# Optimization experiments

Measured on AMD Instinct MI355X. Metric: run time of the kernel, lower is better.

Reference implementation:

```python
import jax, jax.numpy as jnp
import numpy as np
from jax import lax

N_IN, N_H = 3, 2
N_REC = N_IN + N_H  # 5 qubits in the recurrent cell


def _ry(theta):
    # theta: (B,) -> (B, 2, 2) complex64 RY matrices
    c = jnp.cos(theta * 0.5).astype(jnp.complex64)
    s = jnp.sin(theta * 0.5).astype(jnp.complex64)
    return jnp.stack([jnp.stack([c, -s], -1), jnp.stack([s, c], -1)], -2)


def _rot(phi, theta, omega):
    # PennyLane Rot(phi, theta, omega) = RZ(omega) @ RY(theta) @ RZ(phi)
    c = jnp.cos(theta * 0.5)
    s = jnp.sin(theta * 0.5)
    ep = jnp.exp(-0.5j * (phi + omega))  # e^{-i(phi+omega)/2}
    em = jnp.exp(0.5j * (phi - omega))   # e^{+i(phi-omega)/2}
    m = jnp.stack([jnp.stack([ep * c, -em * s], -1),
                   jnp.stack([jnp.conj(em) * s, jnp.conj(ep) * c], -1)], -2)
    return m.astype(jnp.complex64)


def _apply1q(state, U, wire, n):
    # state: (B, 2**n); wire 0 is most significant (PennyLane convention)
    L, R = 2 ** wire, 2 ** (n - wire - 1)
    st = state.reshape(-1, L, 2, R)
    sub = 'bij,bljr->blir' if U.ndim == 3 else 'ij,bljr->blir'
    return jnp.einsum(sub, U, st).reshape(state.shape)


def _cnot_perm(c, t, n):
    # CNOT is a fixed basis permutation: flip target bit where control bit set
    cbit, tbit = 1 << (n - 1 - c), 1 << (n - 1 - t)
    idx = np.arange(2 ** n)
    return np.where(idx & cbit, idx ^ tbit, idx)


def _entangle(state, weights, n):
    # StronglyEntanglingLayers: per-wire Rot, then CNOT ring with range r
    n_layers = weights.shape[0]
    for l in range(n_layers):
        for w in range(n):
            state = _apply1q(state, _rot(weights[l, w, 0], weights[l, w, 1], weights[l, w, 2]), w, n)
        r = (l % (n - 1)) + 1
        for w in range(n):
            state = state[:, _cnot_perm(w, (w + r) % n, n)]
    return state


def _expz(state, wire, n):
    # <Z_wire> = P(0) - P(1)
    L, R = 2 ** wire, 2 ** (n - wire - 1)
    p = (state.real ** 2 + state.imag ** 2).reshape(-1, L, 2, R).sum((1, 3))
    return p[:, 0] - p[:, 1]


def _init_state(batch, n):
    s = jnp.zeros((batch, 2 ** n), jnp.complex64)
    return s.at[:, 0].set(1.0)


def _cell(x, h, w_rec):
    # batched qrnn_cell: RY-encode x on wires 0..2, h on wires 3..4, entangle, read Z(3),Z(4)
    state = _init_state(x.shape[0], N_REC)
    for i in range(N_IN):
        state = _apply1q(state, _ry(x[:, i]), i, N_REC)
    for j in range(N_H):
        state = _apply1q(state, _ry(h[:, j]), N_IN + j, N_REC)
    state = _entangle(state, w_rec, N_REC)
    return jnp.stack([_expz(state, N_IN + j, N_REC) for j in range(N_H)], -1)


def _readout(h, w_out):
    # batched qnn_readout: 2-qubit circuit, Z(0) expval
    state = _init_state(h.shape[0], N_H)
    for j in range(N_H):
        state = _apply1q(state, _ry(h[:, j]), j, N_H)
    state = _entangle(state, w_out, N_H)
    return _expz(state, 0, N_H)[:, None]


def setup_inputs() -> dict:
    key = jax.random.key(0)
    k1, k2, k3 = jax.random.split(key, 3)
    T, B = 32, 8192
    x_seq = jax.random.normal(k1, (T, B, N_IN), jnp.float32)
    w_rec = jax.random.normal(k2, (2, N_REC, 3), jnp.float32)
    w_out = jax.random.normal(k3, (2, N_H, 3), jnp.float32)
    return {"x_seq": x_seq, "w_rec": w_rec, "w_out": w_out}


def reference(x_seq, w_rec, w_out):
    B = x_seq.shape[1]

    def step(h, xt):
        return _cell(xt, h, w_rec), None

    h, _ = lax.scan(step, jnp.zeros((B, N_H), jnp.float32), x_seq)
    return _readout(h, w_out)  # (B, 1)
```

## Files before the change

### kernel.cpp

```cpp
#include <hip/hip_runtime.h>
#include <math.h>


using f32x2 = __attribute__((ext_vector_type(2))) float;
using f32x4 = __attribute__((ext_vector_type(4))) float;

constexpr int cnot_ct(int idx, int c, int t) {
    return (idx & (1 << (4 - c))) ? (idx ^ (1 << (4 - t))) : idx;
}
constexpr int Pfwd_ct(int x, int r) {
    for (int w = 4; w >= 0; --w) x = cnot_ct(x, w, (w + r) % 5);
    return x;
}
constexpr int Pinv_ct(int x, int r) {
    for (int w = 0; w <= 4; ++w) x = cnot_ct(x, w, (w + r) % 5);
    return x;
}
static_assert(Pinv_ct(Pfwd_ct(13, 1), 1) == 13, "inv1");
static_assert(Pinv_ct(Pfwd_ct(22, 2), 2) == 22, "inv2");

constexpr int GMASK[10] = {16, 8, 4, 2, 1,
                           Pfwd_ct(16,1), Pfwd_ct(8,1), Pfwd_ct(4,1), Pfwd_ct(2,1), Pfwd_ct(1,1)};
constexpr int fmask_l1(int pb) {
    int f = 0;
    for (int b = 0; b < 5; ++b) if ((Pinv_ct(1 << b, 1) >> pb) & 1) f |= 1 << b;
    return f;
}
constexpr int FMASK[10] = {16, 8, 4, 2, 1,
                           fmask_l1(4), fmask_l1(3), fmask_l1(2), fmask_l1(1), fmask_l1(0)};
constexpr int cinv_ct(int x) { return Pinv_ct(Pinv_ct(x, 1), 2); }
constexpr int fmask_fin(int pb) {
    int f = 0;
    for (int b = 0; b < 5; ++b) if ((cinv_ct(1 << b) >> pb) & 1) f |= 1 << b;
    return f;
}
constexpr int SF3 = fmask_fin(1);
constexpr int SF4 = fmask_fin(0);

constexpr bool gates_straddle() {
    for (int g = 0; g < 10; ++g)
        if (!(__builtin_popcount(GMASK[g] & FMASK[g]) & 1)) return false;
    return true;
}
static_assert(gates_straddle(), "GMASK/FMASK straddle");

constexpr unsigned span3_ct(int a, int b, int c) {
    unsigned m = 0;
    for (int i = 0; i < 8; ++i) {
        int v = ((i & 1) ? a : 0) ^ ((i & 2) ? b : 0) ^ ((i & 4) ? c : 0);
        m |= 1u << v;
    }
    return m;
}
static_assert(span3_ct(1, 2, 7) == 0xFFu, "butterfly {1,2,7} spans lanes 0..7");

__device__ __forceinline__ int pinv_rt(int x, int r) {
    #pragma unroll
    for (int w = 0; w < 5; ++w) {
        int cbit = 1 << (4 - w), tbit = 1 << (4 - ((w + r) % 5));
        if (x & cbit) x ^= tbit;
    }
    return x;
}

__device__ __forceinline__ float Wsel(int r, int d) {
    float b, c;
    if (d == 0)      { b =  2.f / 3.f; c = 0.f; }
    else if (d == 1) { b = -1.f / 3.f; c =  0.57735026918962576f; }
    else             { b = -1.f / 3.f; c = -0.57735026918962576f; }
    return (r == 0) ? (1.f / 3.f) : ((r == 1) ? b : c);
}

__device__ __forceinline__ float f4c(const float4& v, int c) {
    return (c == 0) ? v.x : ((c == 1) ? v.y : ((c == 2) ? v.z : v.w));
}

__device__ __forceinline__ f32x2 pkfma(f32x2 a, f32x2 b, f32x2 c) {
    return __builtin_elementwise_fma(a, b, c);
}
__device__ __forceinline__ f32x2 splat2(float v) { return (f32x2){v, v}; }

template<int CTRL> __device__ __forceinline__ float dppf(float x) {
    return __int_as_float(__builtin_amdgcn_mov_dpp(__float_as_int(x), CTRL, 0xF, 0xF, true));
}
template<int PL> __device__ __forceinline__ float mvf(float x) {
    if constexpr (PL == 1)      return dppf<0xB1>(x);
    else if constexpr (PL == 2) return dppf<0x4E>(x);
    else if constexpr (PL == 7) return dppf<0x141>(x);
    else if constexpr (PL == 8) return dppf<0x128>(x);
    else { static_assert(PL == 1 || PL == 2 || PL == 7 || PL == 8, "mask"); return x; }
}

template<int g>
__device__ __forceinline__ void gate_full2(f32x2 (&amp)[32], f32x2 cc, f32x2 ss) {
    constexpr int m = GMASK[g], F = FMASK[g];
    #pragma unroll
    for (int i = 0; i < 32; ++i) {
        if ((__builtin_popcount(i & F) & 1) == 0) {
            const int j = i ^ m;
            const f32x2 v0 = amp[i], v1 = amp[j];
            amp[i] = pkfma(cc, v0, -(ss * v1));
            amp[j] = pkfma(ss, v0,  cc * v1);
        }
    }
}

__global__ __launch_bounds__(512, 2) void qrnn_fused(
    const float* __restrict__ x_seq, const float* __restrict__ w_rec,
    const float* __restrict__ w_out, float* __restrict__ out, int B) {

    __shared__ __align__(16) float4 xs4[32 * 33];
    __shared__ __align__(16) float A2s[18 * 28];
    __shared__ float CgS[10], SgS[10];
    __shared__ float F0c[5], F0s[5];
    __shared__ __align__(8) f32x2 E1cs[32];
    __shared__ float RC[16];
    __shared__ __align__(16) float Cm_pool[32 * 18 * 36];
    float* const Qs  = Cm_pool;
    float* const P1s = Cm_pool + 512;

    const int tloc = threadIdx.x;
    const int grp  = tloc >> 4;
    const int k    = tloc & 15;
    const int b0   = blockIdx.x * 32;
    const int b    = b0 + grp;

    #pragma unroll
    for (int qq = 0; qq < 2; ++qq) {
        const int p = tloc + qq * 512;
        const int ts = p >> 5, lbs = p & 31;
        const int gidx = (ts * B + (b0 + lbs)) * 3;
        float4 v;
        v.x = x_seq[gidx]; v.y = x_seq[gidx + 1]; v.z = x_seq[gidx + 2]; v.w = 0.f;
        xs4[lbs * 33 + ts] = v;
    }

    if (tloc < 10) {
        const float th = w_rec[(tloc / 5) * 15 + (tloc % 5) * 3 + 1];
        CgS[tloc] = cosf(0.5f * th);
        SgS[tloc] = sinf(0.5f * th);
    } else if (tloc >= 16 && tloc < 21) {
        const int w = tloc - 16;
        const float ph = 0.5f * w_rec[w * 3 + 0];
        F0c[w] = cosf(ph); F0s[w] = sinf(ph);
    } else if (tloc >= 64 && tloc < 96) {
        const int i = tloc - 64;
        const int j = pinv_rt(i, 1);
        float ang = 0.f;
        #pragma unroll
        for (int w = 0; w < 5; ++w) {
            ang += (((i >> (4 - w)) & 1) ? 0.5f : -0.5f) * w_rec[w * 3 + 2];
            ang += (((j >> (4 - w)) & 1) ? 0.5f : -0.5f) * w_rec[15 + w * 3 + 0];
        }
        E1cs[i] = (f32x2){cosf(ang), sinf(ang)};
    } else if (tloc >= 96 && tloc < 100) {
        const int g = tloc - 96;
        const int li = g >> 1, w = g & 1;
        const float phi = w_out[li * 6 + w * 3 + 0];
        const float the = w_out[li * 6 + w * 3 + 1];
        const float ome = w_out[li * 6 + w * 3 + 2];
        const float cs = cosf(0.5f * the), ss = sinf(0.5f * the);
        const float cp = cosf(0.5f * (phi + ome)), sp = sinf(0.5f * (phi + ome));
        const float cm = cosf(0.5f * (phi - ome)), sm = sinf(0.5f * (phi - ome));
        RC[g * 4 + 0] = cp * cs;
        RC[g * 4 + 1] = -sp * cs;
        RC[g * 4 + 2] = cm * ss;
        RC[g * 4 + 3] = sm * ss;
    }
    __syncthreads();

    if (tloc < 243) {
        const int dsel[5] = {tloc / 81, (tloc / 27) % 3, (tloc / 9) % 3,
                             (tloc / 3) % 3, tloc % 3};
        constexpr float S3v = 0.86602540378443865f;
        float Arw[5], Aiw[5], Brw[5], Biw[5];
        #pragma unroll
        for (int w = 0; w < 5; ++w) {
            const int d = dsel[w];
            const float fc = (d == 0) ? 1.f : 0.5f;
            const float fs = (d == 0) ? 0.f : ((d == 1) ? S3v : -S3v);
            const float c = CgS[w], s = SgS[w];
            const float t1 = fmaf(c, fc, -s * fs);
            const float t2 = fmaf(c, fc,  s * fs);
            const float t3 = fmaf(s, fc,  c * fs);
            const float t4 = fmaf(c, fs, -s * fc);
            Arw[w] =  F0c[w] * t1;  Aiw[w] = -F0s[w] * t2;
            Brw[w] =  F0c[w] * t3;  Biw[w] =  F0s[w] * t4;
        }
        f32x2 amp[32];
        amp[0] = (f32x2){Arw[0], Aiw[0]};
        amp[1] = (f32x2){Brw[0], Biw[0]};
        #pragma unroll
        for (int w = 1; w < 5; ++w) {
            const int n = 1 << w;
            #pragma unroll
            for (int m = n - 1; m >= 0; --m) {
                const float orr = amp[m].x, oii = amp[m].y;
                amp[2*m]   = (f32x2){fmaf(orr, Arw[w], -oii * Aiw[w]),
                                     fmaf(orr, Aiw[w],  oii * Arw[w])};
                amp[2*m+1] = (f32x2){fmaf(orr, Brw[w], -oii * Biw[w]),
                                     fmaf(orr, Biw[w],  oii * Brw[w])};
            }
        }
        #pragma unroll
        for (int i = 0; i < 32; ++i) {
            const f32x2 e = E1cs[i];
            const f32x2 a = amp[i];
            amp[i] = (f32x2){a.x * e.x - a.y * e.y, a.x * e.y + a.y * e.x};
        }
        {
            const f32x2 c5 = splat2(CgS[5]), s5 = splat2(SgS[5]);
            const f32x2 c6 = splat2(CgS[6]), s6 = splat2(SgS[6]);
            const f32x2 c7 = splat2(CgS[7]), s7 = splat2(SgS[7]);
            const f32x2 c8 = splat2(CgS[8]), s8 = splat2(SgS[8]);
            const f32x2 c9 = splat2(CgS[9]), s9 = splat2(SgS[9]);
            gate_full2<5>(amp, c5, s5);
            gate_full2<6>(amp, c6, s6);
            gate_full2<7>(amp, c7, s7);
            gate_full2<8>(amp, c8, s8);
            gate_full2<9>(amp, c9, s9);
        }
        float q0 = 0.f, q1 = 0.f;
        #pragma unroll
        for (int i = 0; i < 32; ++i) {
            const f32x2 t = amp[i] * amp[i];
            const float p = t.x + t.y;
            q0 += (__builtin_popcount(i & SF3) & 1) ? -p : p;
            q1 += (__builtin_popcount(i & SF4) & 1) ? -p : p;
        }
        *(f32x2*)&Qs[tloc * 2] = (f32x2){q0, q1};
    }
    __syncthreads();

    if (tloc < 243) {
        const int e = tloc;
        const int d012 = e / 9, pq = e % 9, pp = pq / 3, qq2 = pq % 3;
        f32x2 acc = (f32x2){0.f, 0.f};
        #pragma unroll
        for (int d3 = 0; d3 < 3; ++d3) {
            const float wp = Wsel(pp, d3);
            #pragma unroll
            for (int d4 = 0; d4 < 3; ++d4) {
                const float w = wp * Wsel(qq2, d4);
                const f32x2 qp = *(const f32x2*)&Qs[(d012 * 9 + d3 * 3 + d4) * 2];
                acc = pkfma(splat2(w), qp, acc);
            }
        }
        *(f32x2*)&P1s[(d012 * 9 + pq) * 2] = acc;
    }
    __syncthreads();

    if (tloc < 243) {
        const int pq = tloc / 27, col = tloc % 27;
        const int a0 = col / 9, a1 = (col / 3) % 3, a2 = col % 3;
        f32x2 acc = (f32x2){0.f, 0.f};
        #pragma unroll
        for (int dd0 = 0; dd0 < 3; ++dd0) {
            const float w0 = Wsel(a0, dd0);
            #pragma unroll
            for (int dd1 = 0; dd1 < 3; ++dd1) {
                const float w01 = w0 * Wsel(a1, dd1);
                #pragma unroll
                for (int dd2 = 0; dd2 < 3; ++dd2) {
                    const float w = w01 * Wsel(a2, dd2);
                    const f32x2 pp = *(const f32x2*)
                        &P1s[((dd0 * 9 + dd1 * 3 + dd2) * 9 + pq) * 2];
                    acc = pkfma(splat2(w), pp, acc);
                }
            }
        }
        A2s[pq * 28 + col]       = acc.x;
        A2s[(9 + pq) * 28 + col] = acc.y;
    }
    if (tloc < 18) A2s[tloc * 28 + 27] = 0.f;
    __syncthreads();

    constexpr float Kf = 0.15915494309189535f;
    const f32x4* Ap = (const f32x4*)A2s;
    f32x4 bA[7], bB[7];
    #pragma unroll
    for (int i = 0; i < 7; ++i) bA[i] = Ap[i];
    #pragma unroll
    for (int i = 0; i < 7; ++i) bB[i] = Ap[7 + i];

    f32x2 Xp0[14], Xp1[14];
    #pragma unroll
    for (int tt = 0; tt < 2; ++tt) {
        float Xb[28];
        const float4 xv = xs4[grp * 33 + k + 16 * tt];
        const float cx0 = __builtin_amdgcn_cosf(xv.x * Kf);
        const float sx0 = __builtin_amdgcn_cosf(fmaf(xv.x, Kf, -0.25f));
        const float cx1 = __builtin_amdgcn_cosf(xv.y * Kf);
        const float sx1 = __builtin_amdgcn_cosf(fmaf(xv.y, Kf, -0.25f));
        const float cx2 = __builtin_amdgcn_cosf(xv.z * Kf);
        const float sx2 = __builtin_amdgcn_cosf(fmaf(xv.z, Kf, -0.25f));
        Xb[0] = 1.f;  Xb[1] = cx2;       Xb[2] = sx2;
        Xb[3] = cx1;  Xb[4] = cx1 * cx2; Xb[5] = cx1 * sx2;
        Xb[6] = sx1;  Xb[7] = sx1 * cx2; Xb[8] = sx1 * sx2;
        #pragma unroll
        for (int i = 0; i < 9; ++i) { Xb[9 + i] = cx0 * Xb[i]; Xb[18 + i] = sx0 * Xb[i]; }
        Xb[27] = 0.f;
        #pragma unroll
        for (int j = 0; j < 14; ++j) {
            const f32x2 pr = (f32x2){Xb[2 * j], Xb[2 * j + 1]};
            if (tt == 0) Xp0[j] = pr; else Xp1[j] = pr;
        }
    }
    {
        float* const Cmg = Cm_pool + grp * (18 * 36);
        #pragma unroll 1
        for (int r = 0; r < 18; r += 2) {
            {
                f32x2 A00 = {0.f,0.f}, A01 = {0.f,0.f}, A10 = {0.f,0.f}, A11 = {0.f,0.f};
                #pragma unroll
                for (int i = 0; i < 7; ++i) {
                    const f32x2 lo = __builtin_shufflevector(bA[i], bA[i], 0, 1);
                    const f32x2 hi = __builtin_shufflevector(bA[i], bA[i], 2, 3);
                    A00 = pkfma(lo, Xp0[2*i],   A00);
                    A01 = pkfma(hi, Xp0[2*i+1], A01);
                    A10 = pkfma(lo, Xp1[2*i],   A10);
                    A11 = pkfma(hi, Xp1[2*i+1], A11);
                }
                const f32x2 S0 = A00 + A01, S1 = A10 + A11;
                Cmg[r * 36 + k]      = S0.x + S0.y;
                Cmg[r * 36 + k + 16] = S1.x + S1.y;
                if (r < 16) {
                    #pragma unroll
                    for (int i = 0; i < 7; ++i) bA[i] = Ap[(r + 2) * 7 + i];
                }
            }
            {
                f32x2 A00 = {0.f,0.f}, A01 = {0.f,0.f}, A10 = {0.f,0.f}, A11 = {0.f,0.f};
                #pragma unroll
                for (int i = 0; i < 7; ++i) {
                    const f32x2 lo = __builtin_shufflevector(bB[i], bB[i], 0, 1);
                    const f32x2 hi = __builtin_shufflevector(bB[i], bB[i], 2, 3);
                    A00 = pkfma(lo, Xp0[2*i],   A00);
                    A01 = pkfma(hi, Xp0[2*i+1], A01);
                    A10 = pkfma(lo, Xp1[2*i],   A10);
                    A11 = pkfma(hi, Xp1[2*i+1], A11);
                }
                const f32x2 S0 = A00 + A01, S1 = A10 + A11;
                Cmg[(r + 1) * 36 + k]      = S0.x + S0.y;
                Cmg[(r + 1) * 36 + k + 16] = S1.x + S1.y;
                if (r < 16) {
                    #pragma unroll
                    for (int i = 0; i < 7; ++i) bB[i] = Ap[(r + 3) * 7 + i];
                }
            }
        }
    }

    const int jj = k >> 3;
    const int term = (k & 7) + 1;
    const int rowA = jj * 9 + term;
    const int rowB = (k == 8) ? 9 : 0;
    const float cbf = (k == 0 || k == 8) ? 1.f : 0.f;
    const int p = term / 3, q = term % 3;
    const float4* CA4 = (const float4*)(Cm_pool + grp * (18 * 36) + rowA * 36);
    const float4* CB4 = (const float4*)(Cm_pool + grp * (18 * 36) + rowB * 36);

    float4 qa[8], qb[8];
    #pragma unroll
    for (int i = 0; i < 8; ++i) { qa[i] = CA4[i]; qb[i] = CB4[i]; }
    #pragma unroll
    for (int i = 0; i < 8; ++i) {
        qb[i].x *= cbf; qb[i].y *= cbf; qb[i].z *= cbf; qb[i].w *= cbf;
    }

    const float Kfu = (p == 0) ? 0.f : Kf;
    const float bu  = (p == 2) ? -0.25f : 0.f;
    const float Kfv = (q == 0) ? 0.f : Kf;
    const float bv  = (q == 2) ? -0.25f : 0.f;

    float h0 = 0.f, h1 = 0.f;
    #pragma unroll
    for (int t = 0; t < 32; ++t) {
        const float u = __builtin_amdgcn_cosf(fmaf(h0, Kfu, bu));
        const float v = __builtin_amdgcn_cosf(fmaf(h1, Kfv, bv));
        float val = fmaf(f4c(qa[t >> 2], t & 3), u * v, f4c(qb[t >> 2], t & 3));
        val += mvf<1>(val);
        val += mvf<2>(val);
        val += mvf<7>(val);
        const float other = mvf<8>(val);
        h0 = (k & 8) ? other : val;
        h1 = (k & 8) ? val : other;
    }

    constexpr float K2 = 0.5f * 0.15915494309189535f;
    const float ch0 = __builtin_amdgcn_cosf(h0 * K2);
    const float sh0 = __builtin_amdgcn_cosf(fmaf(h0, K2, -0.25f));
    const float ch1 = __builtin_amdgcn_cosf(h1 * K2);
    const float sh1 = __builtin_amdgcn_cosf(fmaf(h1, K2, -0.25f));
    float vr0 = ch0 * ch1, vr1 = ch0 * sh1, vr2 = sh0 * ch1, vr3 = sh0 * sh1;
    float vi0 = 0.f, vi1 = 0.f, vi2 = 0.f, vi3 = 0.f;

    #pragma unroll
    for (int li = 0; li < 2; ++li) {
        #pragma unroll
        for (int w = 0; w < 2; ++w) {
            const int g = li * 2 + w;
            const float are = RC[g*4+0], aim = RC[g*4+1];
            const float bre = RC[g*4+2], bim = RC[g*4+3];
            #define AP2(r0, i0, r1, i1) do {                                  \
                float n0r = are*(r0) - aim*(i0) - bre*(r1) + bim*(i1);        \
                float n0i = are*(i0) + aim*(r0) - bre*(i1) - bim*(r1);        \
                float n1r = bre*(r0) + bim*(i0) + are*(r1) + aim*(i1);        \
                float n1i = bre*(i0) - bim*(r0) + are*(i1) - aim*(r1);        \
                r0 = n0r; i0 = n0i; r1 = n1r; i1 = n1i; } while (0)
            if (w == 0) { AP2(vr0, vi0, vr2, vi2); AP2(vr1, vi1, vr3, vi3); }
            else        { AP2(vr0, vi0, vr1, vi1); AP2(vr2, vi2, vr3, vi3); }
            #undef AP2
        }
        float tr1 = vr2, ti1 = vi2, tr2 = vr3, ti2 = vi3, tr3 = vr1, ti3 = vi1;
        vr1 = tr1; vi1 = ti1; vr2 = tr2; vi2 = ti2; vr3 = tr3; vi3 = ti3;
    }

    const float outv = (vr0 * vr0 + vi0 * vi0 + vr1 * vr1 + vi1 * vi1) -
                       (vr2 * vr2 + vi2 * vi2 + vr3 * vr3 + vi3 * vi3);
    if (k == 0) out[b] = outv;
}

extern "C" void kernel_launch(void* const* d_in, const int* in_sizes, int n_in,
                              void* d_out, int out_size, void* d_ws, size_t ws_size,
                              hipStream_t stream) {
    const float* x_seq = (const float*)d_in[0];
    const float* w_rec = (const float*)d_in[1];
    const float* w_out = (const float*)d_in[2];
    float* out = (float*)d_out;

    const int B = out_size;
    const int grid = B / 32;

    hipLaunchKernelGGL(qrnn_fused, dim3(grid), dim3(512), 0, stream,
                       x_seq, w_rec, w_out, out, B);
}
```

Before: 69.30 us.

## Assign 32 threads per batch element and halve block batch to 16

Each block now handles 16 batch elements with 32 threads each, so every thread handles one timestep in the precompute GEMV instead of two. Shared memory for the x tile and Cm pool is halved, and launch bounds are raised to target 4 blocks per CU. The grid doubles. This cuts per-thread register pressure and serial work in the precompute phase and is meant to raise occupancy. The cost is more blocks, each repeating the per-block setup (weight trig, A2s build). The later stages still index with k = l&15, so half of each 32-lane group may do duplicate work.

Result: slower. 74.38 us (+7.3%).

```diff
diff --git a/kernel.cpp b/kernel.cpp
--- a/kernel.cpp
+++ b/kernel.cpp
@@ -105,30 +105,29 @@
     }
 }
 
-__global__ __launch_bounds__(512, 2) void qrnn_fused(
+__global__ __launch_bounds__(512, 4) void qrnn_fused(
     const float* __restrict__ x_seq, const float* __restrict__ w_rec,
     const float* __restrict__ w_out, float* __restrict__ out, int B) {
 
-    __shared__ __align__(16) float4 xs4[32 * 33];
+    __shared__ __align__(16) float4 xs4[16 * 33];
     __shared__ __align__(16) float A2s[18 * 28];
     __shared__ float CgS[10], SgS[10];
     __shared__ float F0c[5], F0s[5];
     __shared__ __align__(8) f32x2 E1cs[32];
     __shared__ float RC[16];
-    __shared__ __align__(16) float Cm_pool[32 * 18 * 36];
+    __shared__ __align__(16) float Cm_pool[16 * 18 * 36];
     float* const Qs  = Cm_pool;
     float* const P1s = Cm_pool + 512;
 
     const int tloc = threadIdx.x;
-    const int grp  = tloc >> 4;
-    const int k    = tloc & 15;
-    const int b0   = blockIdx.x * 32;
+    const int grp  = tloc >> 5;
+    const int l    = tloc & 31;
+    const int k    = l & 15;
+    const int b0   = blockIdx.x * 16;
     const int b    = b0 + grp;
 
-    #pragma unroll
-    for (int qq = 0; qq < 2; ++qq) {
-        const int p = tloc + qq * 512;
-        const int ts = p >> 5, lbs = p & 31;
+    {
+        const int ts = tloc >> 4, lbs = tloc & 15;
         const int gidx = (ts * B + (b0 + lbs)) * 3;
         float4 v;
         v.x = x_seq[gidx]; v.y = x_seq[gidx + 1]; v.z = x_seq[gidx + 2]; v.w = 0.f;
@@ -283,11 +282,10 @@
     #pragma unroll
     for (int i = 0; i < 7; ++i) bB[i] = Ap[7 + i];
 
-    f32x2 Xp0[14], Xp1[14];
-    #pragma unroll
-    for (int tt = 0; tt < 2; ++tt) {
+    f32x2 Xp[14];
+    {
         float Xb[28];
-        const float4 xv = xs4[grp * 33 + k + 16 * tt];
+        const float4 xv = xs4[grp * 33 + l];
         const float cx0 = __builtin_amdgcn_cosf(xv.x * Kf);
         const float sx0 = __builtin_amdgcn_cosf(fmaf(xv.x, Kf, -0.25f));
         const float cx1 = __builtin_amdgcn_cosf(xv.y * Kf);
@@ -301,48 +299,39 @@
         for (int i = 0; i < 9; ++i) { Xb[9 + i] = cx0 * Xb[i]; Xb[18 + i] = sx0 * Xb[i]; }
         Xb[27] = 0.f;
         #pragma unroll
-        for (int j = 0; j < 14; ++j) {
-            const f32x2 pr = (f32x2){Xb[2 * j], Xb[2 * j + 1]};
-            if (tt == 0) Xp0[j] = pr; else Xp1[j] = pr;
-        }
+        for (int j = 0; j < 14; ++j) Xp[j] = (f32x2){Xb[2 * j], Xb[2 * j + 1]};
     }
     {
         float* const Cmg = Cm_pool + grp * (18 * 36);
         #pragma unroll 1
         for (int r = 0; r < 18; r += 2) {
             {
-                f32x2 A00 = {0.f,0.f}, A01 = {0.f,0.f}, A10 = {0.f,0.f}, A11 = {0.f,0.f};
+                f32x2 A00 = {0.f,0.f}, A01 = {0.f,0.f};
                 #pragma unroll
                 for (int i = 0; i < 7; ++i) {
                     const f32x2 lo = __builtin_shufflevector(bA[i], bA[i], 0, 1);
                     const f32x2 hi = __builtin_shufflevector(bA[i], bA[i], 2, 3);
-                    A00 = pkfma(lo, Xp0[2*i],   A00);
-                    A01 = pkfma(hi, Xp0[2*i+1], A01);
-                    A10 = pkfma(lo, Xp1[2*i],   A10);
-                    A11 = pkfma(hi, Xp1[2*i+1], A11);
+                    A00 = pkfma(lo, Xp[2*i],   A00);
+                    A01 = pkfma(hi, Xp[2*i+1], A01);
                 }
-                const f32x2 S0 = A00 + A01, S1 = A10 + A11;
-                Cmg[r * 36 + k]      = S0.x + S0.y;
-                Cmg[r * 36 + k + 16] = S1.x + S1.y;
+                const f32x2 S = A00 + A01;
+                Cmg[r * 36 + l] = S.x + S.y;
                 if (r < 16) {
                     #pragma unroll
                     for (int i = 0; i < 7; ++i) bA[i] = Ap[(r + 2) * 7 + i];
                 }
             }
             {
-                f32x2 A00 = {0.f,0.f}, A01 = {0.f,0.f}, A10 = {0.f,0.f}, A11 = {0.f,0.f};
+                f32x2 A00 = {0.f,0.f}, A01 = {0.f,0.f};
                 #pragma unroll
                 for (int i = 0; i < 7; ++i) {
                     const f32x2 lo = __builtin_shufflevector(bB[i], bB[i], 0, 1);
                     const f32x2 hi = __builtin_shufflevector(bB[i], bB[i], 2, 3);
-                    A00 = pkfma(lo, Xp0[2*i],   A00);
-                    A01 = pkfma(hi, Xp0[2*i+1], A01);
-                    A10 = pkfma(lo, Xp1[2*i],   A10);
-                    A11 = pkfma(hi, Xp1[2*i+1], A11);
+                    A00 = pkfma(lo, Xp[2*i],   A00);
+                    A01 = pkfma(hi, Xp[2*i+1], A01);
                 }
-                const f32x2 S0 = A00 + A01, S1 = A10 + A11;
-                Cmg[(r + 1) * 36 + k]      = S0.x + S0.y;
-                Cmg[(r + 1) * 36 + k + 16] = S1.x + S1.y;
+                const f32x2 S = A00 + A01;
+                Cmg[(r + 1) * 36 + l] = S.x + S.y;
                 if (r < 16) {
                     #pragma unroll
                     for (int i = 0; i < 7; ++i) bB[i] = Ap[(r + 3) * 7 + i];
@@ -418,7 +407,7 @@
 
     const float outv = (vr0 * vr0 + vi0 * vi0 + vr1 * vr1 + vi1 * vi1) -
                        (vr2 * vr2 + vi2 * vi2 + vr3 * vr3 + vi3 * vi3);
-    if (k == 0) out[b] = outv;
+    if (l == 0) out[b] = outv;
 }
 
 extern "C" void kernel_launch(void* const* d_in, const int* in_sizes, int n_in,
@@ -430,7 +419,7 @@
     float* out = (float*)d_out;
 
     const int B = out_size;
-    const int grid = B / 32;
+    const int grid = B / 16;
 
     hipLaunchKernelGGL(qrnn_fused, dim3(grid), dim3(512), 0, stream,
                        x_seq, w_rec, w_out, out, B);
```
